# Kernel tuning notes

Measured on AMD Instinct MI355X. Metric: run time of the kernel, lower is better.

## Reference

```python
import jax, jax.numpy as jnp
import numpy as np


def setup_inputs() -> dict:
    key = jax.random.key(0)
    k1, k2, k3, k4 = jax.random.split(key, 4)
    B, H, W = 16, 256, 256
    CF = 128  # FeatureDA channels
    return {
        "infeat": jax.random.normal(k1, (B, 2, H, W), jnp.float32),
        "labelTpesudo": jax.random.uniform(k2, (B, 1, H, W), jnp.float32),
        "labelT": jax.random.uniform(k3, (B, 1, H, W), jnp.float32),
        "FeatureDA": jax.random.normal(k4, (B, CF, H, W), jnp.float32),
        "k": 2,
        "size": 32,
    }


def _gather_points(x, bi, yy, xx):
    # x: [B, C, H, W]; bi/yy/xx: [n_cls, B, k] -> [n_cls, B, k, C]
    return x.transpose(0, 2, 3, 1)[bi, yy, xx]


def reference(infeat, labelTpesudo, labelT, FeatureDA, k, size):
    B, C, H, W = infeat.shape  # C = 2 classes
    maxc = H - 1  # orisize - 1
    out = jax.nn.softmax(infeat, axis=1)  # channel softmax (implicit dim=1 for 4D)
    flat = out.reshape(B, C, H * W)
    # torch.topk(k*size*size, sorted=True); only the first k entries are used
    vals, idx = jax.lax.top_k(flat, k * size * size)  # [B, C, k*size*size]
    idx_k = idx[:, :, :k].transpose(1, 0, 2)   # [C, B, k], class-major like the c-loop
    vals_k = vals[:, :, :k].transpose(1, 0, 2)  # [C, B, k]
    # grid_xy: x = flat_index % W, y = flat_index // W
    py = idx_k // W
    px = idx_k % W
    bi = jnp.broadcast_to(jnp.arange(B)[None, :, None], idx_k.shape)
    # each loop iteration gathers a single pixel at (oy[0], ox[0]) = (py, px)
    # (stride=1, padding=0 => max(0, px*1-0) == px)
    classiferT = _gather_points(infeat, bi, py, px).reshape(-1, C)                      # 'ClassiferT'
    patchFeatDA = _gather_points(FeatureDA, bi, py, px).reshape(-1, FeatureDA.shape[1])  # 'patchFeatDA'
    labelTTrue = _gather_points(labelT, bi, py, px).reshape(-1, labelT.shape[1])
    labelpesudo = _gather_points(labelTpesudo, bi, py, px).reshape(-1, labelTpesudo.shape[1])
    provalue = vals_k.reshape(-1, 1)  # values[i, :, j]
    # oxy = [[ox0, ox1], [oy0, oy1]] with hardcoded 32-pixel extent, clamped to orisize-1
    ox = jnp.stack([px, jnp.minimum(px + 32 - 1, maxc)], axis=-1)
    oy = jnp.stack([py, jnp.minimum(py + 32 - 1, maxc)], axis=-1)
    pointXY = jnp.stack([ox, oy], axis=-2).reshape(-1, 2, 2).astype(jnp.int32)
    # concatenation order matches Pixel_select_gen: all unchg (c=0) then chg (c=1)
    return classiferT, patchFeatDA, labelTTrue, labelpesudo, provalue, pointXY
```

## Files before the change

kernel.cpp:

```cpp
#include <hip/hip_runtime.h>
#include <math.h>

static constexpr int Bb   = 16;
static constexpr int Ww   = 256;
static constexpr int HWp  = 256 * 256;
static constexpr int CF   = 128;
static constexpr int Kk   = 2;
static constexpr int SEGS = 8;
static constexpr int SEGLEN = HWp / SEGS;

__device__ __forceinline__ bool better(float v1, int i1, float v2, int i2) {
    return (v1 > v2) || ((v1 == v2) && (i1 < i2));
}

__device__ __forceinline__ void merge2(float& a0, int& ia0, float& a1, int& ia1,
                                       float b0, int ib0, float b1, int ib1) {
    if (better(b0, ib0, a0, ia0)) {
        float na1; int nia1;
        if (better(a0, ia0, b1, ib1)) { na1 = a0; nia1 = ia0; }
        else                          { na1 = b1; nia1 = ib1; }
        a0 = b0; ia0 = ib0; a1 = na1; ia1 = nia1;
    } else if (better(b0, ib0, a1, ia1)) {
        a1 = b0; ia1 = ib0;
    }
}

__global__ __launch_bounds__(256) void top2_partial(
    const float* __restrict__ infeat, float* __restrict__ ws_v, int* __restrict__ ws_i)
{
    const int row = blockIdx.x;
    const int seg = blockIdx.y;
    const int b = row >> 1, c = row & 1;
    const float* x0p = infeat + (size_t)(b * 2 + 0) * HWp;
    const float* x1p = infeat + (size_t)(b * 2 + 1) * HWp;
    const int t = threadIdx.x;

    float v0 = -INFINITY, v1 = -INFINITY;
    int   i0 = 0x7fffffff, i1 = 0x7fffffff;

    const int base = seg * SEGLEN + t * 4;
    #pragma unroll
    for (int it = 0; it < SEGLEN / (256 * 4); ++it) {
        const int p = base + it * (256 * 4);
        const float4 a  = *(const float4*)(x0p + p);
        const float4 bb = *(const float4*)(x1p + p);
        const float ax[4] = {a.x, a.y, a.z, a.w};
        const float bx[4] = {bb.x, bb.y, bb.z, bb.w};
        #pragma unroll
        for (int e = 0; e < 4; ++e) {
            const float m  = fmaxf(ax[e], bx[e]);
            const float e0 = expf(ax[e] - m);
            const float e1 = expf(bx[e] - m);
            const float v  = (c == 0 ? e0 : e1) / (e0 + e1);
            const int p2 = p + e;
            if (better(v, p2, v0, i0)) { v1 = v0; i1 = i0; v0 = v; i0 = p2; }
            else if (better(v, p2, v1, i1)) { v1 = v; i1 = p2; }
        }
    }

    #pragma unroll
    for (int m = 1; m < 64; m <<= 1) {
        float o0 = __shfl_xor(v0, m), o1 = __shfl_xor(v1, m);
        int  oi0 = __shfl_xor(i0, m), oi1 = __shfl_xor(i1, m);
        merge2(v0, i0, v1, i1, o0, oi0, o1, oi1);
    }

    __shared__ float sv[4][2];
    __shared__ int   si[4][2];
    const int wave = t >> 6;
    if ((t & 63) == 0) {
        sv[wave][0] = v0; sv[wave][1] = v1;
        si[wave][0] = i0; si[wave][1] = i1;
    }
    __syncthreads();
    if (t == 0) {
        float a0 = sv[0][0], a1 = sv[0][1];
        int  ia0 = si[0][0], ia1 = si[0][1];
        #pragma unroll
        for (int wv = 1; wv < 4; ++wv) {
            merge2(a0, ia0, a1, ia1, sv[wv][0], si[wv][0], sv[wv][1], si[wv][1]);
        }
        ws_v[(row * SEGS + seg) * 2 + 0] = a0;
        ws_v[(row * SEGS + seg) * 2 + 1] = a1;
        ws_i[(row * SEGS + seg) * 2 + 0] = ia0;
        ws_i[(row * SEGS + seg) * 2 + 1] = ia1;
    }
}

__global__ __launch_bounds__(128) void gather_out(
    const float* __restrict__ infeat,
    const float* __restrict__ labelTpesudo,
    const float* __restrict__ labelT,
    const float* __restrict__ FeatureDA,
    const float* __restrict__ ws_v, const int* __restrict__ ws_i,
    float* __restrict__ out)
{
    const int pi = blockIdx.x;
    const int c  = pi / (Bb * Kk);
    const int b  = (pi / Kk) % Bb;
    const int j  = pi % Kk;
    const int row = b * 2 + c;

    __shared__ float s_val;
    __shared__ int   s_idx;
    if (threadIdx.x == 0) {
        float bv0 = -INFINITY, bv1 = -INFINITY;
        int   bi0 = 0x7fffffff, bi1 = 0x7fffffff;
        for (int s2 = 0; s2 < SEGS; ++s2) {
            #pragma unroll
            for (int e = 0; e < 2; ++e) {
                const float v = ws_v[(row * SEGS + s2) * 2 + e];
                const int   i = ws_i[(row * SEGS + s2) * 2 + e];
                if (better(v, i, bv0, bi0)) { bv1 = bv0; bi1 = bi0; bv0 = v; bi0 = i; }
                else if (better(v, i, bv1, bi1)) { bv1 = v; bi1 = i; }
            }
        }
        s_val = (j == 0) ? bv0 : bv1;
        s_idx = (j == 0) ? bi0 : bi1;
    }
    __syncthreads();

    const int   idx = s_idx;
    const float val = s_val;
    const int py = idx >> 8;
    const int px = idx & (Ww - 1);
    const int t = threadIdx.x;

    out[128 + pi * CF + t] = FeatureDA[((size_t)b * CF + t) * HWp + idx];
    if (t < 2) out[pi * 2 + t] = infeat[((size_t)b * 2 + t) * HWp + idx];
    if (t == 0) {
        out[8320 + pi] = labelT[(size_t)b * HWp + idx];
        out[8384 + pi] = labelTpesudo[(size_t)b * HWp + idx];
        out[8448 + pi] = val;
        out[8512 + pi * 4 + 0] = (float)px;
        out[8512 + pi * 4 + 1] = (float)min(px + 31, 255);
        out[8512 + pi * 4 + 2] = (float)py;
        out[8512 + pi * 4 + 3] = (float)min(py + 31, 255);
    }
}

extern "C" void kernel_launch(void* const* d_in, const int* in_sizes, int n_in,
                              void* d_out, int out_size, void* d_ws, size_t ws_size,
                              hipStream_t stream) {
    const float* infeat       = (const float*)d_in[0];
    const float* labelTpesudo = (const float*)d_in[1];
    const float* labelT       = (const float*)d_in[2];
    const float* FeatureDA    = (const float*)d_in[3];
    float* out = (float*)d_out;

    float* ws_v = (float*)d_ws;
    int*   ws_i = (int*)((char*)d_ws + 32 * SEGS * 2 * sizeof(float));

    dim3 g1(32, SEGS);
    top2_partial<<<g1, 256, 0, stream>>>(infeat, ws_v, ws_i);
    gather_out<<<64, 128, 0, stream>>>(infeat, labelTpesudo, labelT, FeatureDA,
                                       ws_v, ws_i, out);
}
```

Measured before the change: 17.82 us.

## Fuse top-2 search and gather into one cooperative kernel with grid sync

Merges the partial top-2 reduction kernel and the gather kernel into a single cooperative launch of 256 blocks, separated by a grid-wide barrier. The goal is to remove the second kernel launch and the gap between the two stages. In exchange it pays for a grid sync and for cooperative launch overhead, which on AMD can be costly and may cost more than the launch it saves.

After: 50.02 us. 181% more time.

```diff
diff --git a/kernel.cpp b/kernel.cpp
--- a/kernel.cpp
+++ b/kernel.cpp
@@ -1,5 +1,8 @@
 #include <hip/hip_runtime.h>
+#include <hip/hip_cooperative_groups.h>
 #include <math.h>
+
+namespace cg = cooperative_groups;
 
 static constexpr int Bb   = 16;
 static constexpr int Ww   = 256;
@@ -8,6 +11,7 @@
 static constexpr int Kk   = 2;
 static constexpr int SEGS = 8;
 static constexpr int SEGLEN = HWp / SEGS;
+static constexpr int NBLK = 32 * SEGS;
 
 __device__ __forceinline__ bool better(float v1, int i1, float v2, int i2) {
     return (v1 > v2) || ((v1 == v2) && (i1 < i2));
@@ -25,98 +29,101 @@
     }
 }
 
-__global__ __launch_bounds__(256) void top2_partial(
-    const float* __restrict__ infeat, float* __restrict__ ws_v, int* __restrict__ ws_i)
-{
-    const int row = blockIdx.x;
-    const int seg = blockIdx.y;
-    const int b = row >> 1, c = row & 1;
-    const float* x0p = infeat + (size_t)(b * 2 + 0) * HWp;
-    const float* x1p = infeat + (size_t)(b * 2 + 1) * HWp;
-    const int t = threadIdx.x;
-
-    float v0 = -INFINITY, v1 = -INFINITY;
-    int   i0 = 0x7fffffff, i1 = 0x7fffffff;
-
-    const int base = seg * SEGLEN + t * 4;
-    #pragma unroll
-    for (int it = 0; it < SEGLEN / (256 * 4); ++it) {
-        const int p = base + it * (256 * 4);
-        const float4 a  = *(const float4*)(x0p + p);
-        const float4 bb = *(const float4*)(x1p + p);
-        const float ax[4] = {a.x, a.y, a.z, a.w};
-        const float bx[4] = {bb.x, bb.y, bb.z, bb.w};
-        #pragma unroll
-        for (int e = 0; e < 4; ++e) {
-            const float m  = fmaxf(ax[e], bx[e]);
-            const float e0 = expf(ax[e] - m);
-            const float e1 = expf(bx[e] - m);
-            const float v  = (c == 0 ? e0 : e1) / (e0 + e1);
-            const int p2 = p + e;
-            if (better(v, p2, v0, i0)) { v1 = v0; i1 = i0; v0 = v; i0 = p2; }
-            else if (better(v, p2, v1, i1)) { v1 = v; i1 = p2; }
-        }
-    }
-
-    #pragma unroll
-    for (int m = 1; m < 64; m <<= 1) {
-        float o0 = __shfl_xor(v0, m), o1 = __shfl_xor(v1, m);
-        int  oi0 = __shfl_xor(i0, m), oi1 = __shfl_xor(i1, m);
-        merge2(v0, i0, v1, i1, o0, oi0, o1, oi1);
-    }
-
-    __shared__ float sv[4][2];
-    __shared__ int   si[4][2];
-    const int wave = t >> 6;
-    if ((t & 63) == 0) {
-        sv[wave][0] = v0; sv[wave][1] = v1;
-        si[wave][0] = i0; si[wave][1] = i1;
-    }
-    __syncthreads();
-    if (t == 0) {
-        float a0 = sv[0][0], a1 = sv[0][1];
-        int  ia0 = si[0][0], ia1 = si[0][1];
-        #pragma unroll
-        for (int wv = 1; wv < 4; ++wv) {
-            merge2(a0, ia0, a1, ia1, sv[wv][0], si[wv][0], sv[wv][1], si[wv][1]);
-        }
-        ws_v[(row * SEGS + seg) * 2 + 0] = a0;
-        ws_v[(row * SEGS + seg) * 2 + 1] = a1;
-        ws_i[(row * SEGS + seg) * 2 + 0] = ia0;
-        ws_i[(row * SEGS + seg) * 2 + 1] = ia1;
-    }
-}
-
-__global__ __launch_bounds__(128) void gather_out(
+__global__ __launch_bounds__(256) void genpixel_coop(
     const float* __restrict__ infeat,
     const float* __restrict__ labelTpesudo,
     const float* __restrict__ labelT,
     const float* __restrict__ FeatureDA,
-    const float* __restrict__ ws_v, const int* __restrict__ ws_i,
+    float* __restrict__ ws_v, int* __restrict__ ws_i,
     float* __restrict__ out)
 {
-    const int pi = blockIdx.x;
-    const int c  = pi / (Bb * Kk);
-    const int b  = (pi / Kk) % Bb;
-    const int j  = pi % Kk;
-    const int row = b * 2 + c;
+    const int blk = blockIdx.x;
+    const int row = blk >> 3;
+    const int seg = blk & 7;
+    const int b = row >> 1, c = row & 1;
+    const int t = threadIdx.x;
+
+    {
+        const float* x0p = infeat + (size_t)(b * 2 + 0) * HWp;
+        const float* x1p = infeat + (size_t)(b * 2 + 1) * HWp;
+
+        float v0 = -INFINITY, v1 = -INFINITY;
+        int   i0 = 0x7fffffff, i1 = 0x7fffffff;
+
+        const int base = seg * SEGLEN + t * 4;
+        #pragma unroll
+        for (int it = 0; it < SEGLEN / (256 * 4); ++it) {
+            const int p = base + it * (256 * 4);
+            const float4 a  = *(const float4*)(x0p + p);
+            const float4 bb = *(const float4*)(x1p + p);
+            const float ax[4] = {a.x, a.y, a.z, a.w};
+            const float bx[4] = {bb.x, bb.y, bb.z, bb.w};
+            #pragma unroll
+            for (int e = 0; e < 4; ++e) {
+                const float m  = fmaxf(ax[e], bx[e]);
+                const float e0 = expf(ax[e] - m);
+                const float e1 = expf(bx[e] - m);
+                const float v  = (c == 0 ? e0 : e1) / (e0 + e1);
+                const int p2 = p + e;
+                if (better(v, p2, v0, i0)) { v1 = v0; i1 = i0; v0 = v; i0 = p2; }
+                else if (better(v, p2, v1, i1)) { v1 = v; i1 = p2; }
+            }
+        }
+
+        #pragma unroll
+        for (int m = 1; m < 64; m <<= 1) {
+            float o0 = __shfl_xor(v0, m), o1 = __shfl_xor(v1, m);
+            int  oi0 = __shfl_xor(i0, m), oi1 = __shfl_xor(i1, m);
+            merge2(v0, i0, v1, i1, o0, oi0, o1, oi1);
+        }
+
+        __shared__ float sv[4][2];
+        __shared__ int   si[4][2];
+        const int wave = t >> 6;
+        if ((t & 63) == 0) {
+            sv[wave][0] = v0; sv[wave][1] = v1;
+            si[wave][0] = i0; si[wave][1] = i1;
+        }
+        __syncthreads();
+        if (t == 0) {
+            float a0 = sv[0][0], a1 = sv[0][1];
+            int  ia0 = si[0][0], ia1 = si[0][1];
+            #pragma unroll
+            for (int wv = 1; wv < 4; ++wv) {
+                merge2(a0, ia0, a1, ia1, sv[wv][0], si[wv][0], sv[wv][1], si[wv][1]);
+            }
+            ws_v[(row * SEGS + seg) * 2 + 0] = a0;
+            ws_v[(row * SEGS + seg) * 2 + 1] = a1;
+            ws_i[(row * SEGS + seg) * 2 + 0] = ia0;
+            ws_i[(row * SEGS + seg) * 2 + 1] = ia1;
+        }
+    }
+
+    cg::this_grid().sync();
+
+    if (blk >= 64) return;
+    const int pi = blk;
+    const int pc = pi / (Bb * Kk);
+    const int pb = (pi / Kk) % Bb;
+    const int pj = pi % Kk;
+    const int prow = pb * 2 + pc;
 
     __shared__ float s_val;
     __shared__ int   s_idx;
-    if (threadIdx.x == 0) {
+    if (t == 0) {
         float bv0 = -INFINITY, bv1 = -INFINITY;
         int   bi0 = 0x7fffffff, bi1 = 0x7fffffff;
         for (int s2 = 0; s2 < SEGS; ++s2) {
             #pragma unroll
             for (int e = 0; e < 2; ++e) {
-                const float v = ws_v[(row * SEGS + s2) * 2 + e];
-                const int   i = ws_i[(row * SEGS + s2) * 2 + e];
+                const float v = ws_v[(prow * SEGS + s2) * 2 + e];
+                const int   i = ws_i[(prow * SEGS + s2) * 2 + e];
                 if (better(v, i, bv0, bi0)) { bv1 = bv0; bi1 = bi0; bv0 = v; bi0 = i; }
                 else if (better(v, i, bv1, bi1)) { bv1 = v; bi1 = i; }
             }
         }
-        s_val = (j == 0) ? bv0 : bv1;
-        s_idx = (j == 0) ? bi0 : bi1;
+        s_val = (pj == 0) ? bv0 : bv1;
+        s_idx = (pj == 0) ? bi0 : bi1;
     }
     __syncthreads();
 
@@ -124,13 +131,13 @@
     const float val = s_val;
     const int py = idx >> 8;
     const int px = idx & (Ww - 1);
-    const int t = threadIdx.x;
 
-    out[128 + pi * CF + t] = FeatureDA[((size_t)b * CF + t) * HWp + idx];
-    if (t < 2) out[pi * 2 + t] = infeat[((size_t)b * 2 + t) * HWp + idx];
+    if (t < CF)
+        out[128 + pi * CF + t] = FeatureDA[((size_t)pb * CF + t) * HWp + idx];
+    if (t < 2) out[pi * 2 + t] = infeat[((size_t)pb * 2 + t) * HWp + idx];
     if (t == 0) {
-        out[8320 + pi] = labelT[(size_t)b * HWp + idx];
-        out[8384 + pi] = labelTpesudo[(size_t)b * HWp + idx];
+        out[8320 + pi] = labelT[(size_t)pb * HWp + idx];
+        out[8384 + pi] = labelTpesudo[(size_t)pb * HWp + idx];
         out[8448 + pi] = val;
         out[8512 + pi * 4 + 0] = (float)px;
         out[8512 + pi * 4 + 1] = (float)min(px + 31, 255);
@@ -151,8 +158,8 @@
     float* ws_v = (float*)d_ws;
     int*   ws_i = (int*)((char*)d_ws + 32 * SEGS * 2 * sizeof(float));
 
-    dim3 g1(32, SEGS);
-    top2_partial<<<g1, 256, 0, stream>>>(infeat, ws_v, ws_i);
-    gather_out<<<64, 128, 0, stream>>>(infeat, labelTpesudo, labelT, FeatureDA,
-                                       ws_v, ws_i, out);
+    void* args[] = { (void*)&infeat, (void*)&labelTpesudo, (void*)&labelT,
+                     (void*)&FeatureDA, (void*)&ws_v, (void*)&ws_i, (void*)&out };
+    hipLaunchCooperativeKernel((const void*)genpixel_coop,
+                               dim3(NBLK), dim3(256), args, 0, stream);
 }
```
